# Optimization experiments

Measured on AMD Instinct MI355X. Metric: run time of the kernel, lower is better.

The kernel has to match this reference:

```python
import jax, jax.numpy as jnp
import numpy as np

B, T, D_IN, Z, H, L = 256, 512, 64, 32, 64, 2
DT, DISC = 0.1, 10

def _u(key, shape, fan):
    b = 1.0 / np.sqrt(fan)
    return jax.random.uniform(key, shape, jnp.float32, -b, b)

def setup_inputs() -> dict:
    key = jax.random.key(0)
    ks = jax.random.split(key, 16)
    return {
        "x": jax.random.normal(ks[0], (B, T, D_IN), jnp.float32),
        # stacked RNN, layer 0: input D_IN -> Z ; layer 1: Z -> Z
        "W_ih0": _u(ks[1], (Z, D_IN), Z), "W_hh0": _u(ks[2], (Z, Z), Z),
        "b_ih0": _u(ks[3], (Z,), Z),      "b_hh0": _u(ks[4], (Z,), Z),
        "W_ih1": _u(ks[5], (Z, Z), Z),    "W_hh1": _u(ks[6], (Z, Z), Z),
        "b_ih1": _u(ks[7], (Z,), Z),      "b_hh1": _u(ks[8], (Z,), Z),
        "h0": jnp.zeros((L, 1, Z), jnp.float32),  # learned initial state, init zeros
        # LatentODEfunc MLP: Z -> H -> H -> Z with ELU
        "fc1_w": _u(ks[9], (H, Z), Z),  "fc1_b": _u(ks[10], (H,), Z),
        "fc2_w": _u(ks[11], (H, H), H), "fc2_b": _u(ks[12], (H,), H),
        "fc3_w": _u(ks[13], (Z, H), H), "fc3_b": _u(ks[14], (Z,), H),
    }

def _rnn(x_rev, layers, h0):
    # x_rev: [B, T, D]; torch nn.RNN (tanh), batch_first, stacked layers
    inp = jnp.swapaxes(x_rev, 0, 1)  # [T, B, D]
    Bsz = x_rev.shape[0]
    for l, (Wi, Wh, bi, bh) in enumerate(layers):
        h_init = jnp.broadcast_to(h0[l], (Bsz, h0.shape[-1]))
        def step(h, xt, Wi=Wi, Wh=Wh, bi=bi, bh=bh):
            h = jnp.tanh(xt @ Wi.T + bi + h @ Wh.T + bh)
            return h, h
        _, inp = jax.lax.scan(step, h_init, inp)
    return jnp.swapaxes(inp, 0, 1)  # [B, T, Z]

def reference(x, W_ih0, W_hh0, b_ih0, b_hh0, W_ih1, W_hh1, b_ih1, b_hh1,
              h0, fc1_w, fc1_b, fc2_w, fc2_b, fc3_w, fc3_b):
    seq_len = x.shape[1]
    # reverse_sequences with full lengths == flip time; RNN; pad_and_reverse == flip back
    x_rev = jnp.flip(x, axis=1)
    layers = [(W_ih0, W_hh0, b_ih0, b_hh0), (W_ih1, W_hh1, b_ih1, b_hh1)]
    rnn_out = jnp.flip(_rnn(x_rev, layers, h0), axis=1)  # [B, T, Z]

    elu = jax.nn.elu
    def f(y):  # autonomous latent ODE vector field (t unused in original)
        return elu(elu(y @ fc1_w.T + fc1_b) @ fc2_w.T + fc2_b) @ fc3_w.T + fc3_b

    # odeint(f, y0, arange(0, dt, dt/disc))[-1]: integrate from 0 to dt*(disc-1)/disc.
    # Fixed-step RK4 on that grid; each timestep's IC is rnn_out[:, t+1] (independent),
    # so integrate all (B, T-1) states at once.
    h_step = DT / DISC
    y0 = rnn_out[:, 1:, :]  # [B, T-1, Z]
    def rk4(y, _):
        k1 = f(y)
        k2 = f(y + 0.5 * h_step * k1)
        k3 = f(y + 0.5 * h_step * k2)
        k4 = f(y + h_step * k3)
        return y + (h_step / 6.0) * (k1 + 2.0 * k2 + 2.0 * k3 + k4), None
    yT, _ = jax.lax.scan(rk4, y0, None, length=DISC - 1)
    # ode_output[:, t] = yT[:, t] for t < T-1; ode_output[:, T-1] = rnn_out[:, T-1]
    return jnp.concatenate([yT, rnn_out[:, -1:, :]], axis=1)
```

## Files before the change

### kernel.cpp

```cpp
#include <hip/hip_runtime.h>
#include <hip/hip_bf16.h>
#include <math.h>

#define BB 256
#define TT 512
#define DIN 64
#define ZZ 32
#define HH 64
#define NITEMS 8192
#define NBAR 513

typedef __attribute__((ext_vector_type(4))) float f32x4;
typedef __attribute__((ext_vector_type(8))) __bf16 bf16x8;
typedef __attribute__((ext_vector_type(4))) __bf16 bf16x4;
typedef __attribute__((ext_vector_type(2))) unsigned int u32x2;
typedef __attribute__((ext_vector_type(4))) unsigned int u32x4;
typedef unsigned long long u64;

union FragU { u32x4 u; bf16x8 b; };
union HalfU { bf16x4 b; u32x2 u; };
union VecU  { f32x4 f; u64 u[2]; };

__device__ __forceinline__ f32x4 mfma16(bf16x8 a, bf16x8 b, f32x4 c) {
  return __builtin_amdgcn_mfma_f32_16x16x32_bf16(a, b, c, 0, 0, 0);
}

__device__ __forceinline__ float elu1(float v) {
  return fminf(v, __expf(v) - 1.f);
}
__device__ __forceinline__ f32x4 elu4(f32x4 v) {
  f32x4 r;
  r.x = elu1(v.x); r.y = elu1(v.y); r.z = elu1(v.z); r.w = elu1(v.w);
  return r;
}

__device__ __forceinline__ bf16x8 pack2(f32x4 a, f32x4 b) {
  bf16x8 r;
  r[0] = (__bf16)a.x; r[1] = (__bf16)a.y; r[2] = (__bf16)a.z; r[3] = (__bf16)a.w;
  r[4] = (__bf16)b.x; r[5] = (__bf16)b.y; r[6] = (__bf16)b.z; r[7] = (__bf16)b.w;
  return r;
}

__device__ __forceinline__ void packhl(f32x4 a, f32x4 b, bf16x8& hi, bf16x8& lo) {
  hi = pack2(a, b);
  f32x4 ra, rb;
  ra.x = (float)hi[0]; ra.y = (float)hi[1]; ra.z = (float)hi[2]; ra.w = (float)hi[3];
  rb.x = (float)hi[4]; rb.y = (float)hi[5]; rb.z = (float)hi[6]; rb.w = (float)hi[7];
  lo = pack2(a - ra, b - rb);
}

__device__ __forceinline__ void packh2(f32x4 v, u32x2& hi, u32x2& lo) {
  HalfU H, L;
  H.b[0] = (__bf16)v.x; H.b[1] = (__bf16)v.y;
  H.b[2] = (__bf16)v.z; H.b[3] = (__bf16)v.w;
  f32x4 r;
  r.x = (float)H.b[0]; r.y = (float)H.b[1];
  r.z = (float)H.b[2]; r.w = (float)H.b[3];
  f32x4 d = v - r;
  L.b[0] = (__bf16)d.x; L.b[1] = (__bf16)d.y;
  L.b[2] = (__bf16)d.z; L.b[3] = (__bf16)d.w;
  hi = H.u; lo = L.u;
}

__device__ __forceinline__ bf16x8 ldw(const float* rowp, int o1, int o2) {
  f32x4 a = *reinterpret_cast<const f32x4*>(rowp + o1);
  f32x4 b = *reinterpret_cast<const f32x4*>(rowp + o2);
  return pack2(a, b);
}
__device__ __forceinline__ void ldw2(const float* rowp, int o1, int o2,
                                     bf16x8& hi, bf16x8& lo) {
  f32x4 a = *reinterpret_cast<const f32x4*>(rowp + o1);
  f32x4 b = *reinterpret_cast<const f32x4*>(rowp + o2);
  packhl(a, b, hi, lo);
}

__device__ __forceinline__ float tanh1(float x) {
  float t = __expf(2.f * x);
  return fmaf(-2.f, __builtin_amdgcn_rcpf(t + 1.f), 1.f);
}
__device__ __forceinline__ f32x4 tanh4(f32x4 v) {
  f32x4 r;
  r.x = tanh1(v.x); r.y = tanh1(v.y); r.z = tanh1(v.z); r.w = tanh1(v.w);
  return r;
}

#define STEP_BARRIER() asm volatile("s_waitcnt lgkmcnt(0)\ns_barrier" ::: "memory")

__device__ __forceinline__ void cp_store8(u64* p, u64 v) {
  __hip_atomic_store(p, v, __ATOMIC_RELAXED, __HIP_MEMORY_SCOPE_AGENT);
}
__device__ __forceinline__ u64 cp_load8(const u64* p) {
  return __hip_atomic_load(p, __ATOMIC_RELAXED, __HIP_MEMORY_SCOPE_AGENT);
}

__device__ __forceinline__ int* chain_flag(float* rnn, int ch) {
  return (int*)(rnn + (size_t)(ch * 16) * TT * ZZ);
}

__global__ __launch_bounds__(256, 2) void prep_kernel(
    const float* __restrict__ x,
    const float* __restrict__ Wi0,
    const float* __restrict__ bi0, const float* __restrict__ bh0,
    float* __restrict__ p0, float* __restrict__ rnn)
{
  if (blockIdx.x == 0) {
    const int t = threadIdx.x;
    if (t < 16) *chain_flag(rnn, t) = 0;
    if (t == 16) *((int*)(rnn + (size_t)TT * ZZ)) = 0;
  }
  const int lane = threadIdx.x & 63;
  const int wv = threadIdx.x >> 6;
  const int q = lane >> 4, c = lane & 15;

  bf16x8 Wh[2][2], Wl[2][2];
  #pragma unroll
  for (int kt = 0; kt < 2; ++kt)
    #pragma unroll
    for (int mt = 0; mt < 2; ++mt)
      ldw2(Wi0 + (16 * mt + c) * 64, 32 * kt + 4 * q, 32 * kt + 16 + 4 * q,
           Wh[kt][mt], Wl[kt][mt]);
  f32x4 B0[2];
  #pragma unroll
  for (int mt = 0; mt < 2; ++mt)
    B0[mt] = *reinterpret_cast<const f32x4*>(bi0 + 16 * mt + 4 * q) +
             *reinterpret_cast<const f32x4*>(bh0 + 16 * mt + 4 * q);

  const unsigned row = blockIdx.x * 64u + (unsigned)wv * 16u + (unsigned)c;
  const float* xp = x + (size_t)row * DIN;
  f32x4 x0 = *reinterpret_cast<const f32x4*>(xp + 4 * q);
  f32x4 x1 = *reinterpret_cast<const f32x4*>(xp + 16 + 4 * q);
  f32x4 x2 = *reinterpret_cast<const f32x4*>(xp + 32 + 4 * q);
  f32x4 x3 = *reinterpret_cast<const f32x4*>(xp + 48 + 4 * q);
  bf16x8 xf0 = pack2(x0, x1), xf1 = pack2(x2, x3);

  float* pout = p0 + (size_t)row * ZZ;
  #pragma unroll
  for (int mt = 0; mt < 2; ++mt) {
    f32x4 a = mfma16(Wh[0][mt], xf0, B0[mt]);
    a = mfma16(Wl[0][mt], xf0, a);
    a = mfma16(Wh[1][mt], xf1, a);
    a = mfma16(Wl[1][mt], xf1, a);
    *reinterpret_cast<f32x4*>(pout + 16 * mt + 4 * q) = a;
  }
}

__global__ __launch_bounds__(512, 1) void fused_kernel(
    const float* __restrict__ p0buf,
    const float* __restrict__ Wh0,
    const float* __restrict__ Wi1, const float* __restrict__ Wh1,
    const float* __restrict__ bi1, const float* __restrict__ bh1,
    const float* __restrict__ h0g,
    const float* __restrict__ w1, const float* __restrict__ b1,
    const float* __restrict__ w2, const float* __restrict__ b2,
    const float* __restrict__ w3, const float* __restrict__ b3,
    float* __restrict__ rnn, float* __restrict__ out)
{
  __shared__ __align__(16) unsigned int sh[2][4][256];
  const int lane = threadIdx.x & 63;
  const int wv = threadIdx.x >> 6;
  const int q = lane >> 4, c = lane & 15;
  const f32x4 Z4 = {0.f, 0.f, 0.f, 0.f};

  if (blockIdx.x < 16) {
    if (wv >= 4) {
      for (int i = 0; i < NBAR; ++i) STEP_BARRIER();
      return;
    }
    __builtin_amdgcn_s_setprio(1);
    const int ch = blockIdx.x;
    const int b0 = ch * 16;

    const float* pp = p0buf + (size_t)(b0 + c) * TT * ZZ;
    float* pr = rnn + (size_t)(b0 + c) * TT * ZZ;
    float* po = out + (size_t)(b0 + c) * TT * ZZ;
    int* flg = chain_flag(rnn, ch);

    const int mt = wv & 1;
    const int dwoff = lane * 4 + mt * 2;

    if (wv < 2) {
      bf16x8 W0h, W0l;
      ldw2(Wh0 + (16 * mt + c) * 32, 4 * q, 16 + 4 * q, W0h, W0l);
      const float* ppt = pp + 16 * mt + 4 * q;

      {
        f32x4 u = *reinterpret_cast<const f32x4*>(h0g + 16 * mt + 4 * q);
        u32x2 hi, lo;
        packh2(u, hi, lo);
        *reinterpret_cast<u32x2*>(&sh[0][0][dwoff]) = hi;
        *reinterpret_cast<u32x2*>(&sh[0][1][dwoff]) = lo;
      }
      f32x4 Pa = *reinterpret_cast<const f32x4*>(ppt + (size_t)511 * ZZ);
      f32x4 Pb = *reinterpret_cast<const f32x4*>(ppt + (size_t)510 * ZZ);
      f32x4 Pc = *reinterpret_cast<const f32x4*>(ppt + (size_t)509 * ZZ);

      STEP_BARRIER();

      auto DSTEP = [&](int s, f32x4& Pm) {
        const int cur = s & 1;
        FragU z0, z1;
        z0.u = *reinterpret_cast<const u32x4*>(&sh[cur][0][lane * 4]);
        z1.u = *reinterpret_cast<const u32x4*>(&sh[cur][1][lane * 4]);
        f32x4 dm = mfma16(W0h, z0.b, Pm);
        f32x4 dl = mfma16(W0l, z0.b, mfma16(W0h, z1.b, Z4));
        {
          const int t = 511 - s;
          const int tl = t >= 3 ? t - 3 : 0;
          Pm = *reinterpret_cast<const f32x4*>(ppt + (size_t)tl * ZZ);
        }
        f32x4 d = tanh4(dm + dl);
        u32x2 hi, lo;
        packh2(d, hi, lo);
        *reinterpret_cast<u32x2*>(&sh[cur ^ 1][0][dwoff]) = hi;
        *reinterpret_cast<u32x2*>(&sh[cur ^ 1][1][dwoff]) = lo;
        STEP_BARRIER();
      };

      DSTEP(0, Pa);
      #pragma unroll 1
      for (int g = 0; g < 170; ++g) {
        DSTEP(1 + 3 * g, Pb);
        DSTEP(2 + 3 * g, Pc);
        DSTEP(3 + 3 * g, Pa);
      }
      DSTEP(511, Pb);
    } else {
      bf16x8 W1h0, W1l0, W1h1, W1l1;
      ldw2(Wi1 + (16 * mt + c) * 32, 4 * q, 16 + 4 * q, W1h0, W1l0);
      ldw2(Wh1 + (16 * mt + c) * 32, 4 * q, 16 + 4 * q, W1h1, W1l1);
      f32x4 B1 = *reinterpret_cast<const f32x4*>(bi1 + 16 * mt + 4 * q) +
                 *reinterpret_cast<const f32x4*>(bh1 + 16 * mt + 4 * q);

      STEP_BARRIER();

      {
        f32x4 u = *reinterpret_cast<const f32x4*>(h0g + 32 + 16 * mt + 4 * q);
        u32x2 hi, lo;
        packh2(u, hi, lo);
        *reinterpret_cast<u32x2*>(&sh[1][2][dwoff]) = hi;
        *reinterpret_cast<u32x2*>(&sh[1][3][dwoff]) = lo;
        STEP_BARRIER();
      }

      auto ESTEP = [&](int s) {
        const int cur = s & 1;
        FragU zh0, zl0, zh1, zl1;
        zh0.u = *reinterpret_cast<const u32x4*>(&sh[cur][0][lane * 4]);
        zl0.u = *reinterpret_cast<const u32x4*>(&sh[cur][1][lane * 4]);
        zh1.u = *reinterpret_cast<const u32x4*>(&sh[cur][2][lane * 4]);
        zl1.u = *reinterpret_cast<const u32x4*>(&sh[cur][3][lane * 4]);
        f32x4 ea = mfma16(W1h1, zh1.b, mfma16(W1h0, zh0.b, B1));
        f32x4 eb = mfma16(W1h1, zl1.b, mfma16(W1h0, zl0.b, Z4));
        f32x4 ec = mfma16(W1l1, zh1.b, mfma16(W1l0, zh0.b, Z4));
        f32x4 e = tanh4(ea + (eb + ec));
        const int t = 511 - s;
        {
          VecU cv; cv.f = e;
          u64* dp = reinterpret_cast<u64*>(
              pr + (size_t)(t + 1) * ZZ + 16 * mt + 4 * q);
          cp_store8(dp, cv.u[0]);
          cp_store8(dp + 1, cv.u[1]);
        }
        if (t == 510) {
          float* pot = po + (size_t)511 * ZZ + 16 * mt + 4 * q;
          *reinterpret_cast<f32x4*>(pot) = e;
        }
        u32x2 hi, lo;
        packh2(e, hi, lo);
        *reinterpret_cast<u32x2*>(&sh[cur ^ 1][2][dwoff]) = hi;
        *reinterpret_cast<u32x2*>(&sh[cur ^ 1][3][dwoff]) = lo;
        const bool upd = ((s & 15) == 0) || (s == 511);
        if (upd) asm volatile("s_waitcnt vmcnt(0)" ::: "memory");
        STEP_BARRIER();
        if (upd && mt == 0 && lane == 0)
          __hip_atomic_store(flg, s, __ATOMIC_RELAXED,
                             __HIP_MEMORY_SCOPE_AGENT);
      };

      #pragma unroll 1
      for (int g = 0; g < 170; ++g) {
        ESTEP(1 + 3 * g);
        ESTEP(2 + 3 * g);
        ESTEP(3 + 3 * g);
      }
      ESTEP(511);
    }
    return;
  }

  bf16x8 W1[4], W2[2][4], W3[2][2];
  f32x4 BZ1[4], BZ2[4], BZ3[2];
  #pragma unroll
  for (int mt = 0; mt < 4; ++mt) {
    W1[mt] = ldw(w1 + (16 * mt + c) * 32, 4 * q, 16 + 4 * q);
    BZ1[mt] = *reinterpret_cast<const f32x4*>(b1 + 16 * mt + 4 * q);
    BZ2[mt] = *reinterpret_cast<const f32x4*>(b2 + 16 * mt + 4 * q);
  }
  #pragma unroll
  for (int kt = 0; kt < 2; ++kt)
    #pragma unroll
    for (int mt = 0; mt < 4; ++mt)
      W2[kt][mt] = ldw(w2 + (16 * mt + c) * 64, 32 * kt + 4 * q, 32 * kt + 16 + 4 * q);
  #pragma unroll
  for (int kt = 0; kt < 2; ++kt)
    #pragma unroll
    for (int mt = 0; mt < 2; ++mt)
      W3[kt][mt] = ldw(w3 + (16 * mt + c) * 64, 32 * kt + 4 * q, 32 * kt + 16 + 4 * q);
  #pragma unroll
  for (int mt = 0; mt < 2; ++mt)
    BZ3[mt] = *reinterpret_cast<const f32x4*>(b3 + 16 * mt + 4 * q);

  auto feval = [&](bf16x8 xf, f32x4& o0, f32x4& o1) {
    f32x4 a[4];
    #pragma unroll
    for (int mt = 0; mt < 4; ++mt) a[mt] = mfma16(W1[mt], xf, BZ1[mt]);
    #pragma unroll
    for (int mt = 0; mt < 4; ++mt) a[mt] = elu4(a[mt]);
    bf16x8 h10 = pack2(a[0], a[1]), h11 = pack2(a[2], a[3]);
    f32x4 g[4];
    #pragma unroll
    for (int mt = 0; mt < 4; ++mt)
      g[mt] = mfma16(W2[1][mt], h11, mfma16(W2[0][mt], h10, BZ2[mt]));
    #pragma unroll
    for (int mt = 0; mt < 4; ++mt) g[mt] = elu4(g[mt]);
    bf16x8 h20 = pack2(g[0], g[1]), h21 = pack2(g[2], g[3]);
    o0 = mfma16(W3[1][0], h21, mfma16(W3[0][0], h20, BZ3[0]));
    o1 = mfma16(W3[1][1], h21, mfma16(W3[0][1], h20, BZ3[1]));
  };

  int* ctr = (int*)(rnn + (size_t)TT * ZZ);
  const float hs = 0.01f;

  for (;;) {
    int n0 = 0;
    if (lane == 0)
      n0 = __hip_atomic_fetch_add(ctr, 1, __ATOMIC_RELAXED,
                                  __HIP_MEMORY_SCOPE_AGENT);
    const int n = __shfl(n0, 0);
    if (n >= NITEMS) break;

    const int k7 = n >> 10;
    const int rem = n & 1023;
    const int bb = rem >> 2;
    const int widx = rem & 3;
    const int tp = 510 - (64 * k7 + 16 * widx + c);
    const int ch = bb >> 4;
    int need = 16 + 64 * k7 + 16 * widx;
    if (need > 511) need = 511;

    int* flg = chain_flag(rnn, ch);
    while (__hip_atomic_load(flg, __ATOMIC_RELAXED,
                             __HIP_MEMORY_SCOPE_AGENT) < need)
      __builtin_amdgcn_s_sleep(32);

    const int tpc = tp < 0 ? 0 : tp;
    const u64* sp = reinterpret_cast<const u64*>(
        rnn + ((size_t)bb * TT + tpc + 1) * ZZ);
    VecU c0, c1;
    c0.u[0] = cp_load8(sp + 2 * q);
    c0.u[1] = cp_load8(sp + 2 * q + 1);
    c1.u[0] = cp_load8(sp + 8 + 2 * q);
    c1.u[1] = cp_load8(sp + 8 + 2 * q + 1);
    f32x4 y0 = c0.f;
    f32x4 y1 = c1.f;

    f32x4 k0, k1, ks0, ks1;
    #pragma unroll 1
    for (int it = 0; it < 9; ++it) {
      feval(pack2(y0, y1), k0, k1);
      ks0 = k0; ks1 = k1;
      feval(pack2(y0 + (0.5f * hs) * k0, y1 + (0.5f * hs) * k1), k0, k1);
      ks0 += 2.f * k0; ks1 += 2.f * k1;
      feval(pack2(y0 + (0.5f * hs) * k0, y1 + (0.5f * hs) * k1), k0, k1);
      ks0 += 2.f * k0; ks1 += 2.f * k1;
      feval(pack2(y0 + hs * k0, y1 + hs * k1), k0, k1);
      y0 += (hs / 6.f) * (ks0 + k0);
      y1 += (hs / 6.f) * (ks1 + k1);
    }

    if (tp >= 0) {
      float* dstp = out + ((size_t)bb * TT + tp) * ZZ;
      *reinterpret_cast<f32x4*>(dstp + 4 * q) = y0;
      *reinterpret_cast<f32x4*>(dstp + 16 + 4 * q) = y1;
    }
  }
}

extern "C" void kernel_launch(void* const* d_in, const int* in_sizes, int n_in,
                              void* d_out, int out_size, void* d_ws, size_t ws_size,
                              hipStream_t stream) {
  const float* x   = (const float*)d_in[0];
  const float* Wi0 = (const float*)d_in[1];
  const float* Wh0 = (const float*)d_in[2];
  const float* bi0 = (const float*)d_in[3];
  const float* bh0 = (const float*)d_in[4];
  const float* Wi1 = (const float*)d_in[5];
  const float* Wh1 = (const float*)d_in[6];
  const float* bi1 = (const float*)d_in[7];
  const float* bh1 = (const float*)d_in[8];
  const float* h0  = (const float*)d_in[9];
  const float* w1  = (const float*)d_in[10];
  const float* b1  = (const float*)d_in[11];
  const float* w2  = (const float*)d_in[12];
  const float* b2  = (const float*)d_in[13];
  const float* w3  = (const float*)d_in[14];
  const float* b3  = (const float*)d_in[15];
  float* out = (float*)d_out;
  float* rnn = (float*)d_ws;
  float* p0  = (float*)d_out;

  prep_kernel<<<2048, 256, 0, stream>>>(x, Wi0, bi0, bh0, p0, rnn);
  fused_kernel<<<256, 512, 0, stream>>>(p0, Wh0, Wi1, Wh1, bi1, bh1, h0,
                                        w1, b1, w2, b2, w3, b3, rnn, out);
}
```

Measured before the change: 228.6 us.

## Batch ODE work claims per block and relax RNN progress-flag waits

The layer-0 recurrence now prefetches its precomputed input projections six steps ahead instead of three, using six rotating registers. The layer-1 chain no longer drains all outstanding stores before each progress-flag update. It waits only down to 32 pending stores, publishes a flag lagged by 8 steps, and publishes the final value after a full drain. ODE consumer blocks now claim 8 items at once through a single thread, which spins on the dependency flags and hands the items to the 8 waves through shared memory with block barriers. This cuts atomic traffic and per-wave polling, but all waves in a block now wait for the slowest item and for the block barriers. The lagged flag's correctness depends on the vmcnt bound matching the number of stores issued in the last 8 steps.

```diff
diff --git a/kernel.cpp b/kernel.cpp
--- a/kernel.cpp
+++ b/kernel.cpp
@@ -156,6 +156,7 @@
     float* __restrict__ rnn, float* __restrict__ out)
 {
   __shared__ __align__(16) unsigned int sh[2][4][256];
+  __shared__ int nb_sh;
   const int lane = threadIdx.x & 63;
   const int wv = threadIdx.x >> 6;
   const int q = lane >> 4, c = lane & 15;
@@ -193,6 +194,9 @@
       f32x4 Pa = *reinterpret_cast<const f32x4*>(ppt + (size_t)511 * ZZ);
       f32x4 Pb = *reinterpret_cast<const f32x4*>(ppt + (size_t)510 * ZZ);
       f32x4 Pc = *reinterpret_cast<const f32x4*>(ppt + (size_t)509 * ZZ);
+      f32x4 Pd = *reinterpret_cast<const f32x4*>(ppt + (size_t)508 * ZZ);
+      f32x4 Pe = *reinterpret_cast<const f32x4*>(ppt + (size_t)507 * ZZ);
+      f32x4 Pf = *reinterpret_cast<const f32x4*>(ppt + (size_t)506 * ZZ);
 
       STEP_BARRIER();
 
@@ -205,7 +209,7 @@
         f32x4 dl = mfma16(W0l, z0.b, mfma16(W0h, z1.b, Z4));
         {
           const int t = 511 - s;
-          const int tl = t >= 3 ? t - 3 : 0;
+          const int tl = t >= 6 ? t - 6 : 0;
           Pm = *reinterpret_cast<const f32x4*>(ppt + (size_t)tl * ZZ);
         }
         f32x4 d = tanh4(dm + dl);
@@ -218,10 +222,13 @@
 
       DSTEP(0, Pa);
       #pragma unroll 1
-      for (int g = 0; g < 170; ++g) {
-        DSTEP(1 + 3 * g, Pb);
-        DSTEP(2 + 3 * g, Pc);
-        DSTEP(3 + 3 * g, Pa);
+      for (int g = 0; g < 85; ++g) {
+        DSTEP(1 + 6 * g, Pb);
+        DSTEP(2 + 6 * g, Pc);
+        DSTEP(3 + 6 * g, Pd);
+        DSTEP(4 + 6 * g, Pe);
+        DSTEP(5 + 6 * g, Pf);
+        DSTEP(6 + 6 * g, Pa);
       }
       DSTEP(511, Pb);
     } else {
@@ -269,11 +276,11 @@
         packh2(e, hi, lo);
         *reinterpret_cast<u32x2*>(&sh[cur ^ 1][2][dwoff]) = hi;
         *reinterpret_cast<u32x2*>(&sh[cur ^ 1][3][dwoff]) = lo;
-        const bool upd = ((s & 15) == 0) || (s == 511);
-        if (upd) asm volatile("s_waitcnt vmcnt(0)" ::: "memory");
+        const bool upd = ((s & 15) == 0);
+        if (upd) asm volatile("s_waitcnt vmcnt(32)" ::: "memory");
         STEP_BARRIER();
         if (upd && mt == 0 && lane == 0)
-          __hip_atomic_store(flg, s, __ATOMIC_RELAXED,
+          __hip_atomic_store(flg, s - 8, __ATOMIC_RELAXED,
                              __HIP_MEMORY_SCOPE_AGENT);
       };
 
@@ -284,6 +291,10 @@
         ESTEP(3 + 3 * g);
       }
       ESTEP(511);
+      asm volatile("s_waitcnt vmcnt(0)" ::: "memory");
+      if (mt == 0 && lane == 0)
+        __hip_atomic_store(flg, 511, __ATOMIC_RELAXED,
+                           __HIP_MEMORY_SCOPE_AGENT);
     }
     return;
   }
@@ -332,57 +343,68 @@
   const float hs = 0.01f;
 
   for (;;) {
-    int n0 = 0;
-    if (lane == 0)
-      n0 = __hip_atomic_fetch_add(ctr, 1, __ATOMIC_RELAXED,
-                                  __HIP_MEMORY_SCOPE_AGENT);
-    const int n = __shfl(n0, 0);
-    if (n >= NITEMS) break;
-
-    const int k7 = n >> 10;
-    const int rem = n & 1023;
-    const int bb = rem >> 2;
-    const int widx = rem & 3;
-    const int tp = 510 - (64 * k7 + 16 * widx + c);
-    const int ch = bb >> 4;
-    int need = 16 + 64 * k7 + 16 * widx;
-    if (need > 511) need = 511;
-
-    int* flg = chain_flag(rnn, ch);
-    while (__hip_atomic_load(flg, __ATOMIC_RELAXED,
-                             __HIP_MEMORY_SCOPE_AGENT) < need)
-      __builtin_amdgcn_s_sleep(32);
-
-    const int tpc = tp < 0 ? 0 : tp;
-    const u64* sp = reinterpret_cast<const u64*>(
-        rnn + ((size_t)bb * TT + tpc + 1) * ZZ);
-    VecU c0, c1;
-    c0.u[0] = cp_load8(sp + 2 * q);
-    c0.u[1] = cp_load8(sp + 2 * q + 1);
-    c1.u[0] = cp_load8(sp + 8 + 2 * q);
-    c1.u[1] = cp_load8(sp + 8 + 2 * q + 1);
-    f32x4 y0 = c0.f;
-    f32x4 y1 = c1.f;
-
-    f32x4 k0, k1, ks0, ks1;
-    #pragma unroll 1
-    for (int it = 0; it < 9; ++it) {
-      feval(pack2(y0, y1), k0, k1);
-      ks0 = k0; ks1 = k1;
-      feval(pack2(y0 + (0.5f * hs) * k0, y1 + (0.5f * hs) * k1), k0, k1);
-      ks0 += 2.f * k0; ks1 += 2.f * k1;
-      feval(pack2(y0 + (0.5f * hs) * k0, y1 + (0.5f * hs) * k1), k0, k1);
-      ks0 += 2.f * k0; ks1 += 2.f * k1;
-      feval(pack2(y0 + hs * k0, y1 + hs * k1), k0, k1);
-      y0 += (hs / 6.f) * (ks0 + k0);
-      y1 += (hs / 6.f) * (ks1 + k1);
+    if (threadIdx.x == 0) {
+      int nb = __hip_atomic_fetch_add(ctr, 8, __ATOMIC_RELAXED,
+                                      __HIP_MEMORY_SCOPE_AGENT);
+      nb_sh = nb;
+      #pragma unroll 1
+      for (int i = 0; i < 8; ++i) {
+        const int n = nb + i;
+        if (n >= NITEMS) break;
+        const int k7 = n >> 10;
+        const int bb2 = (n & 1023) >> 2;
+        const int wx = n & 3;
+        int nd = 16 + 64 * k7 + 16 * wx;
+        if (nd > 511) nd = 511;
+        int* flg = chain_flag(rnn, bb2 >> 4);
+        while (__hip_atomic_load(flg, __ATOMIC_RELAXED,
+                                 __HIP_MEMORY_SCOPE_AGENT) < nd)
+          __builtin_amdgcn_s_sleep(64);
+      }
     }
-
-    if (tp >= 0) {
-      float* dstp = out + ((size_t)bb * TT + tp) * ZZ;
-      *reinterpret_cast<f32x4*>(dstp + 4 * q) = y0;
-      *reinterpret_cast<f32x4*>(dstp + 16 + 4 * q) = y1;
+    __syncthreads();
+    const int n = nb_sh + wv;
+    if (nb_sh >= NITEMS) break;
+
+    if (n < NITEMS) {
+      const int k7 = n >> 10;
+      const int rem = n & 1023;
+      const int bb = rem >> 2;
+      const int widx = rem & 3;
+      const int tp = 510 - (64 * k7 + 16 * widx + c);
+
+      const int tpc = tp < 0 ? 0 : tp;
+      const u64* sp = reinterpret_cast<const u64*>(
+          rnn + ((size_t)bb * TT + tpc + 1) * ZZ);
+      VecU c0, c1;
+      c0.u[0] = cp_load8(sp + 2 * q);
+      c0.u[1] = cp_load8(sp + 2 * q + 1);
+      c1.u[0] = cp_load8(sp + 8 + 2 * q);
+      c1.u[1] = cp_load8(sp + 8 + 2 * q + 1);
+      f32x4 y0 = c0.f;
+      f32x4 y1 = c1.f;
+
+      f32x4 k0, k1, ks0, ks1;
+      #pragma unroll 1
+      for (int it = 0; it < 9; ++it) {
+        feval(pack2(y0, y1), k0, k1);
+        ks0 = k0; ks1 = k1;
+        feval(pack2(y0 + (0.5f * hs) * k0, y1 + (0.5f * hs) * k1), k0, k1);
+        ks0 += 2.f * k0; ks1 += 2.f * k1;
+        feval(pack2(y0 + (0.5f * hs) * k0, y1 + (0.5f * hs) * k1), k0, k1);
+        ks0 += 2.f * k0; ks1 += 2.f * k1;
+        feval(pack2(y0 + hs * k0, y1 + hs * k1), k0, k1);
+        y0 += (hs / 6.f) * (ks0 + k0);
+        y1 += (hs / 6.f) * (ks1 + k1);
+      }
+
+      if (tp >= 0) {
+        float* dstp = out + ((size_t)bb * TT + tp) * ZZ;
+        *reinterpret_cast<f32x4*>(dstp + 4 * q) = y0;
+        *reinterpret_cast<f32x4*>(dstp + 16 + 4 * q) = y1;
+      }
     }
+    __syncthreads();
   }
 }
 
```

Result: no change. 226.6 us (-0.9%).
